# Optimization experiments

Hardware: AMD Instinct MI355X
Metric: run time of the kernel (lower is better)

The kernel has to match this reference:

```python
import jax, jax.numpy as jnp
import numpy as np

B, L1, Q_DIM, V_DIM = 4, 4096, 256, 256
NH, NL, NP = 8, 4, 4
LEVELS = [(128, 128), (64, 64), (32, 32), (16, 16)]
L2 = sum(h * w for h, w in LEVELS)  # 21760


def setup_inputs() -> dict:
    key = jax.random.key(0)
    ks = jax.random.split(key, 12)
    xav = lambda k, so, si: jax.random.normal(k, (so, si), jnp.float32) * np.sqrt(2.0 / (so + si)).astype(np.float32)
    # reference windows: centers in [0.1,0.9], box sizes in [0.05,0.25]
    c = 0.1 + 0.8 * jax.random.uniform(ks[0], (B, L1, 2), jnp.float32)
    s = 0.05 + 0.2 * jax.random.uniform(ks[1], (B, L1, 2), jnp.float32)
    v_shape = jnp.array(LEVELS, dtype=jnp.int32)
    v_start_index = jnp.array(np.cumsum([0] + [h * w for h, w in LEVELS[:-1]]), dtype=jnp.int32)
    return {
        'query': jax.random.normal(ks[2], (B, L1, Q_DIM), jnp.float32),
        'value': jax.random.normal(ks[3], (B, L2, V_DIM), jnp.float32),
        'v_shape': v_shape,
        'v_mask': jnp.zeros((B, L2), jnp.bool_),
        'v_start_index': v_start_index,
        'v_valid_ratios': jnp.ones((B, 1, 1, NL, 1, 2), jnp.float32),
        'ref_windows': jnp.concatenate([c, s], axis=-1),
        'Wo': 0.01 * jax.random.normal(ks[4], (NH * NL * NP * 2, Q_DIM), jnp.float32),
        'bo': 0.5 * jax.random.normal(ks[5], (NH * NL * NP * 2,), jnp.float32),
        'Wa': 0.02 * jax.random.normal(ks[6], (NH * NL * NP, Q_DIM), jnp.float32),
        'ba': jnp.zeros((NH * NL * NP,), jnp.float32),
        'Wv': xav(ks[7], V_DIM, V_DIM),
        'bv': jnp.zeros((V_DIM,), jnp.float32),
        'Wout': xav(ks[8], Q_DIM, V_DIM),
        'bout': jnp.zeros((Q_DIM,), jnp.float32),
    }


def _ms_deform_sample(value, v_shape, v_start, loc):
    """value: (b,l2,h,d); loc: (b,l1,h,L,P,2) in [0,1] -> (b,l1,L,P,h,d).
    Bilinear sampling with zero padding, align_corners=False semantics."""
    b, l2, h, d = value.shape
    _, l1, _, L, P, _ = loc.shape
    Hi = v_shape[:, 0][None, None, None, :, None]  # (1,1,1,L,1) int
    Wi = v_shape[:, 1][None, None, None, :, None]
    x = loc[..., 0] * Wi.astype(loc.dtype) - 0.5  # (b,l1,h,L,P)
    y = loc[..., 1] * Hi.astype(loc.dtype) - 0.5
    x0 = jnp.floor(x)
    y0 = jnp.floor(y)
    lx, ly = x - x0, y - y0
    x0i = x0.astype(jnp.int32)
    y0i = y0.astype(jnp.int32)
    start = v_start[None, None, None, :, None]
    acc = jnp.zeros((b, l1 * L * P, h, d), loc.dtype)
    for dy, wy in ((0, 1.0 - ly), (1, ly)):
        for dx, wx in ((0, 1.0 - lx), (1, lx)):
            xi = x0i + dx
            yi = y0i + dy
            valid = (xi >= 0) & (xi < Wi) & (yi >= 0) & (yi < Hi)
            w = wx * wy * valid.astype(loc.dtype)  # (b,l1,h,L,P)
            xc = jnp.clip(xi, 0, Wi - 1)
            yc = jnp.clip(yi, 0, Hi - 1)
            flat = start + yc * Wi + xc  # (b,l1,h,L,P) index into l2
            flat_t = flat.transpose(0, 1, 3, 4, 2).reshape(b, l1 * L * P, h)
            w_t = w.transpose(0, 1, 3, 4, 2).reshape(b, l1 * L * P, h)
            g = jnp.take_along_axis(value, flat_t[..., None], axis=1)  # (b,M,h,d)
            acc = acc + g * w_t[..., None]
    return acc.reshape(b, l1, L, P, h, d)


def reference(query, value, v_shape, v_mask, v_start_index, v_valid_ratios, ref_windows,
              Wo, bo, Wa, ba, Wv, bv, Wout, bout):
    b, l1, _ = query.shape
    l2 = value.shape[1]
    hd = value.shape[-1] // NH
    v = value @ Wv.T + bv
    v = jnp.where(v_mask[..., None], 0.0, v).reshape(b, l2, NH, hd)
    off = (query @ Wo.T + bo).reshape(b, l1, NH, NL, NP, 2)
    attn = jax.nn.softmax((query @ Wa.T + ba).reshape(b, l1, NH, NL * NP), axis=-1)
    attn = attn.reshape(b, l1, NH, NL, NP)
    loc = ref_windows[:, :, None, None, None, :2] + off / 8.0 * ref_windows[:, :, None, None, None, 2:]
    loc = loc * v_valid_ratios
    sampled = _ms_deform_sample(v, v_shape, v_start_index, loc)  # (b,l1,L,P,h,d)
    out = jnp.einsum('blLPhd,blhLP->blhd', sampled, attn).reshape(b, l1, NH * hd)
    out = out @ Wout.T + bout
    return out, attn
```

## Files before the change

### kernel.cpp

```cpp
#include <hip/hip_runtime.h>
#include <cstdint>
#include <cstddef>


#define L2_LEN 21760
#define BQ_TOT 16384
#define KD     256

typedef __attribute__((ext_vector_type(8))) _Float16 half8;
typedef __attribute__((ext_vector_type(4))) float    f32x4;

__device__ __forceinline__ void glds16(const _Float16* g, _Float16* l) {
    __builtin_amdgcn_global_load_lds(
        (const __attribute__((address_space(1))) void*)g,
        (__attribute__((address_space(3))) void*)l, 16, 0, 0);
}

__global__ __launch_bounds__(256) void cvt_f32_f16(
    const float* __restrict__ in, _Float16* __restrict__ out, int n8)
{
    for (int i = blockIdx.x * 256 + threadIdx.x; i < n8; i += gridDim.x * 256) {
        const float4 f0 = ((const float4*)in)[i * 2];
        const float4 f1 = ((const float4*)in)[i * 2 + 1];
        half8 h;
        h[0] = (_Float16)f0.x; h[1] = (_Float16)f0.y;
        h[2] = (_Float16)f0.z; h[3] = (_Float16)f0.w;
        h[4] = (_Float16)f1.x; h[5] = (_Float16)f1.y;
        h[6] = (_Float16)f1.z; h[7] = (_Float16)f1.w;
        ((half8*)out)[i] = h;
    }
}

__global__ __launch_bounds__(256) void cvt_weights(
    const float* __restrict__ Wv, const float* __restrict__ Wo,
    const float* __restrict__ Wa, const float* __restrict__ Wout,
    const float* __restrict__ bv, const float* __restrict__ bo,
    const float* __restrict__ ba, const float* __restrict__ bout,
    _Float16* __restrict__ Wp, float* __restrict__ bp)
{
    const int gid = blockIdx.x * 256 + threadIdx.x;
    const float* src; int off8;
    if      (gid <  8192) { src = Wv;   off8 = gid;         }
    else if (gid < 16384) { src = Wo;   off8 = gid -  8192; }
    else if (gid < 20480) { src = Wa;   off8 = gid - 16384; }
    else                  { src = Wout; off8 = gid - 20480; }
    const float4 f0 = ((const float4*)src)[off8 * 2];
    const float4 f1 = ((const float4*)src)[off8 * 2 + 1];
    half8 h;
    h[0] = (_Float16)f0.x; h[1] = (_Float16)f0.y;
    h[2] = (_Float16)f0.z; h[3] = (_Float16)f0.w;
    h[4] = (_Float16)f1.x; h[5] = (_Float16)f1.y;
    h[6] = (_Float16)f1.z; h[7] = (_Float16)f1.w;
    ((half8*)Wp)[gid] = h;
    if (gid < 896) {
        float b;
        if      (gid < 256) b = bv[gid];
        else if (gid < 512) b = bo[gid - 256];
        else if (gid < 640) b = ba[gid - 512];
        else                b = bout[gid - 640];
        bp[gid] = b;
    }
}

template<bool OUT_F16>
__global__ __launch_bounds__(256) void gemm_f16(
    const _Float16* __restrict__ A, const _Float16* __restrict__ Wp,
    const float* __restrict__ bp, int wrow0,
    void* __restrict__ Cv, int ldC, const unsigned char* __restrict__ mask)
{
    __shared__ _Float16 As[4096];
    __shared__ _Float16 Bs[4096];

    const int t = threadIdx.x, lane = t & 63, wid = t >> 6;
    const int wm = wid >> 1, wn = wid & 1;
    const int bm = blockIdx.x, bn = blockIdx.y;

    const int u0 = wid * 128 + lane;
    const int u1 = u0 + 64;
    const int ra0 = ((u0 >> 6) << 4) + (u0 & 15), ca0 = ((u0 >> 4) & 3) * 8;
    const int ra1 = ((u1 >> 6) << 4) + (u1 & 15), ca1 = ((u1 >> 4) & 3) * 8;
    const _Float16* Ag0 = A + (size_t)(bm * 128 + ra0) * KD + ca0;
    const _Float16* Ag1 = A + (size_t)(bm * 128 + ra1) * KD + ca1;
    const _Float16* Wg0 = Wp + (size_t)(wrow0 + bn * 128 + ra0) * KD + ca0;
    const _Float16* Wg1 = Wp + (size_t)(wrow0 + bn * 128 + ra1) * KD + ca1;
    _Float16* Ad0 = &As[wid * 1024];
    _Float16* Ad1 = &As[wid * 1024 + 512];
    _Float16* Bd0 = &Bs[wid * 1024];
    _Float16* Bd1 = &Bs[wid * 1024 + 512];

    f32x4 acc[4][4] = {};

    for (int kk = 0; kk < KD; kk += 32) {
        glds16(Ag0 + kk, Ad0);
        glds16(Ag1 + kk, Ad1);
        glds16(Wg0 + kk, Bd0);
        glds16(Wg1 + kk, Bd1);
        __syncthreads();
        half8 ah[4], bh[4];
#pragma unroll
        for (int x = 0; x < 4; ++x) {
            ah[x] = ((const half8*)As)[(wm * 4 + x) * 64 + lane];
            bh[x] = ((const half8*)Bs)[(wn * 4 + x) * 64 + lane];
        }
#pragma unroll
        for (int m = 0; m < 4; ++m)
#pragma unroll
            for (int n = 0; n < 4; ++n)
                acc[m][n] = __builtin_amdgcn_mfma_f32_16x16x32_f16(
                    ah[m], bh[n], acc[m][n], 0, 0, 0);
        __syncthreads();
    }

    const int rb = bm * 128 + wm * 64, cb = bn * 128 + wn * 64;
    const int cl = lane & 15, rl = (lane >> 4) * 4;
    float bias_n[4];
#pragma unroll
    for (int n = 0; n < 4; ++n) bias_n[n] = bp[wrow0 + cb + n * 16 + cl];
#pragma unroll
    for (int m = 0; m < 4; ++m) {
        float mz[4];
#pragma unroll
        for (int r = 0; r < 4; ++r) {
            const int row = rb + m * 16 + rl + r;
            mz[r] = (mask != nullptr && mask[row]) ? 0.0f : 1.0f;
        }
#pragma unroll
        for (int n = 0; n < 4; ++n) {
            const int col = cb + n * 16 + cl;
#pragma unroll
            for (int r = 0; r < 4; ++r) {
                const int row = rb + m * 16 + rl + r;
                const float val = (acc[m][n][r] + bias_n[n]) * mz[r];
                if (OUT_F16) ((_Float16*)Cv)[(size_t)row * ldC + col] = (_Float16)val;
                else         ((float*)Cv)[(size_t)row * ldC + col] = val;
            }
        }
    }
}

__global__ __launch_bounds__(256) void softmax_kernel(
    const float* __restrict__ logits, int stride,
    float* __restrict__ attn, int total)
{
    const int i = blockIdx.x * blockDim.x + threadIdx.x;
    if (i >= total) return;
    const int q = i >> 3, h = i & 7;
    const float4* p = (const float4*)(logits + (size_t)q * stride + h * 16);
    const float4 v0 = p[0], v1 = p[1], v2 = p[2], v3 = p[3];
    float v[16] = {v0.x, v0.y, v0.z, v0.w, v1.x, v1.y, v1.z, v1.w,
                   v2.x, v2.y, v2.z, v2.w, v3.x, v3.y, v3.z, v3.w};
    float m = v[0];
#pragma unroll
    for (int j = 1; j < 16; ++j) m = fmaxf(m, v[j]);
    float s = 0.0f;
#pragma unroll
    for (int j = 0; j < 16; ++j) { v[j] = __expf(v[j] - m); s += v[j]; }
    const float inv = 1.0f / s;
    float4* o = (float4*)(attn + (size_t)i * 16);
    o[0] = make_float4(v[0] * inv, v[1] * inv, v[2] * inv, v[3] * inv);
    o[1] = make_float4(v[4] * inv, v[5] * inv, v[6] * inv, v[7] * inv);
    o[2] = make_float4(v[8] * inv, v[9] * inv, v[10] * inv, v[11] * inv);
    o[3] = make_float4(v[12] * inv, v[13] * inv, v[14] * inv, v[15] * inv);
}

__global__ __launch_bounds__(128) void sample_f16(
    const _Float16* __restrict__ v,
    const float* __restrict__ qp,
    const float* __restrict__ attn,
    const float* __restrict__ ref,
    const float* __restrict__ vr,
    const int*   __restrict__ vshape,
    const int*   __restrict__ vstart,
    _Float16* __restrict__ sout)
{
    const int t  = threadIdx.x;
    const int q  = blockIdx.x * 4 + (t >> 5);
    const int h  = (t >> 2) & 7;
    const int c0 = (t & 3) * 8;
    const int b  = q >> 12;

    const float4 rw = *(const float4*)(ref + (size_t)q * 4);
    const float* op = qp + (size_t)q * 384 + h * 32;
    const float* ap = attn + (size_t)q * 128 + h * 16;

    float acc[8] = {};

#pragma unroll
    for (int l = 0; l < 4; ++l) {
        const int H = vshape[l * 2 + 0];
        const int W = vshape[l * 2 + 1];
        const int start = vstart[l];
        const float vrx = vr[(b * 4 + l) * 2 + 0];
        const float vry = vr[(b * 4 + l) * 2 + 1];
        const float fW = (float)W, fH = (float)H;
        const _Float16* vb = v + ((size_t)b * L2_LEN + start) * 256 + h * 32 + c0;
#pragma unroll
        for (int p = 0; p < 4; ++p) {
            const float a  = ap[l * 4 + p];
            const float ox = op[(l * 4 + p) * 2 + 0];
            const float oy = op[(l * 4 + p) * 2 + 1];
            const float x = (rw.x + ox * 0.125f * rw.z) * vrx * fW - 0.5f;
            const float y = (rw.y + oy * 0.125f * rw.w) * vry * fH - 0.5f;
            const float x0f = floorf(x), y0f = floorf(y);
            const float fx = x - x0f, fy = y - y0f;
            const int x0 = (int)x0f, y0 = (int)y0f;
            const float wx0 = (x0 >= 0 && x0 < W)         ? (1.0f - fx) : 0.0f;
            const float wx1 = (x0 + 1 >= 0 && x0 + 1 < W) ? fx          : 0.0f;
            const float wy0 = (y0 >= 0 && y0 < H)         ? (1.0f - fy) : 0.0f;
            const float wy1 = (y0 + 1 >= 0 && y0 + 1 < H) ? fy          : 0.0f;
            const int xc0 = min(max(x0, 0), W - 1),     xc1 = min(max(x0 + 1, 0), W - 1);
            const int yc0 = min(max(y0, 0), H - 1),     yc1 = min(max(y0 + 1, 0), H - 1);
            const float w00 = wx0 * wy0 * a, w01 = wx1 * wy0 * a;
            const float w10 = wx0 * wy1 * a, w11 = wx1 * wy1 * a;
            const half8 g00 = *(const half8*)(vb + (size_t)(yc0 * W + xc0) * 256);
            const half8 g01 = *(const half8*)(vb + (size_t)(yc0 * W + xc1) * 256);
            const half8 g10 = *(const half8*)(vb + (size_t)(yc1 * W + xc0) * 256);
            const half8 g11 = *(const half8*)(vb + (size_t)(yc1 * W + xc1) * 256);
#pragma unroll
            for (int j = 0; j < 8; ++j)
                acc[j] += w00 * (float)g00[j] + w01 * (float)g01[j]
                        + w10 * (float)g10[j] + w11 * (float)g11[j];
        }
    }

    half8 o;
#pragma unroll
    for (int j = 0; j < 8; ++j) o[j] = (_Float16)acc[j];
    *(half8*)(sout + (size_t)q * 256 + h * 32 + c0) = o;
}

extern "C" void kernel_launch(void* const* d_in, const int* in_sizes, int n_in,
                              void* d_out, int out_size, void* d_ws, size_t ws_size,
                              hipStream_t stream)
{
    const float*         query    = (const float*)d_in[0];
    const float*         value    = (const float*)d_in[1];
    const int*           v_shape  = (const int*)d_in[2];
    const unsigned char* v_mask   = (const unsigned char*)d_in[3];
    const int*           v_start  = (const int*)d_in[4];
    const float*         v_ratios = (const float*)d_in[5];
    const float*         ref_w    = (const float*)d_in[6];
    const float*         Wo       = (const float*)d_in[7];
    const float*         bo       = (const float*)d_in[8];
    const float*         Wa       = (const float*)d_in[9];
    const float*         ba       = (const float*)d_in[10];
    const float*         Wv       = (const float*)d_in[11];
    const float*         bv       = (const float*)d_in[12];
    const float*         Wout     = (const float*)d_in[13];
    const float*         bout     = (const float*)d_in[14];

    float* out      = (float*)d_out;
    float* attn_out = out + (size_t)BQ_TOT * 256;

    _Float16* Vf = (_Float16*)d_ws;
    _Float16* vh = Vf + (size_t)4 * L2_LEN * 256;
    _Float16* Qf = vh + (size_t)4 * L2_LEN * 256;
    _Float16* Sf = Qf + (size_t)BQ_TOT * 256;
    _Float16* Wp = Sf + (size_t)BQ_TOT * 256;
    float*    bp = (float*)(Wp + 229376);
    float*    qp = bp + 896;

    cvt_f32_f16<<<2048, 256, 0, stream>>>(value, Vf, (4 * L2_LEN * 256) / 8);
    cvt_f32_f16<<<2048, 256, 0, stream>>>(query, Qf, (BQ_TOT * 256) / 8);
    cvt_weights<<<112, 256, 0, stream>>>(Wv, Wo, Wa, Wout, bv, bo, ba, bout, Wp, bp);
    gemm_f16<true><<<dim3(680, 2), 256, 0, stream>>>(
        Vf, Wp, bp, 0, vh, 256, v_mask);
    gemm_f16<false><<<dim3(128, 3), 256, 0, stream>>>(
        Qf, Wp, bp, 256, qp, 384, nullptr);
    softmax_kernel<<<512, 256, 0, stream>>>(qp + 256, 384, attn_out, BQ_TOT * 8);
    sample_f16<<<4096, 128, 0, stream>>>(
        vh, qp, attn_out, ref_w, v_ratios, v_shape, v_start, Sf);
    gemm_f16<false><<<dim3(128, 2), 256, 0, stream>>>(
        Sf, Wp, bp, 640, out, 256, nullptr);
}
```

Measured before the change: 292.8 us.

## Fuse f32-to-f16 conversion into GEMMs, fold softmax into sampler, head-major value layout

Result: faster. 274.5 us (-6.3%).

```diff
diff --git a/kernel.cpp b/kernel.cpp
--- a/kernel.cpp
+++ b/kernel.cpp
@@ -5,7 +5,6 @@
 
 #define L2_LEN 21760
 #define BQ_TOT 16384
-#define KD     256
 
 typedef __attribute__((ext_vector_type(8))) _Float16 half8;
 typedef __attribute__((ext_vector_type(4))) float    f32x4;
@@ -15,20 +14,13 @@
         (const __attribute__((address_space(1))) void*)g,
         (__attribute__((address_space(3))) void*)l, 16, 0, 0);
 }
-
-__global__ __launch_bounds__(256) void cvt_f32_f16(
-    const float* __restrict__ in, _Float16* __restrict__ out, int n8)
-{
-    for (int i = blockIdx.x * 256 + threadIdx.x; i < n8; i += gridDim.x * 256) {
-        const float4 f0 = ((const float4*)in)[i * 2];
-        const float4 f1 = ((const float4*)in)[i * 2 + 1];
-        half8 h;
-        h[0] = (_Float16)f0.x; h[1] = (_Float16)f0.y;
-        h[2] = (_Float16)f0.z; h[3] = (_Float16)f0.w;
-        h[4] = (_Float16)f1.x; h[5] = (_Float16)f1.y;
-        h[6] = (_Float16)f1.z; h[7] = (_Float16)f1.w;
-        ((half8*)out)[i] = h;
-    }
+__device__ __forceinline__ half8 cvt8(float4 a, float4 b) {
+    half8 h;
+    h[0] = (_Float16)a.x; h[1] = (_Float16)a.y;
+    h[2] = (_Float16)a.z; h[3] = (_Float16)a.w;
+    h[4] = (_Float16)b.x; h[5] = (_Float16)b.y;
+    h[6] = (_Float16)b.z; h[7] = (_Float16)b.w;
+    return h;
 }
 
 __global__ __launch_bounds__(256) void cvt_weights(
@@ -46,12 +38,7 @@
     else                  { src = Wout; off8 = gid - 20480; }
     const float4 f0 = ((const float4*)src)[off8 * 2];
     const float4 f1 = ((const float4*)src)[off8 * 2 + 1];
-    half8 h;
-    h[0] = (_Float16)f0.x; h[1] = (_Float16)f0.y;
-    h[2] = (_Float16)f0.z; h[3] = (_Float16)f0.w;
-    h[4] = (_Float16)f1.x; h[5] = (_Float16)f1.y;
-    h[6] = (_Float16)f1.z; h[7] = (_Float16)f1.w;
-    ((half8*)Wp)[gid] = h;
+    ((half8*)Wp)[gid] = cvt8(f0, f1);
     if (gid < 896) {
         float b;
         if      (gid < 256) b = bv[gid];
@@ -62,11 +49,84 @@
     }
 }
 
-template<bool OUT_F16>
-__global__ __launch_bounds__(256) void gemm_f16(
-    const _Float16* __restrict__ A, const _Float16* __restrict__ Wp,
+__global__ __launch_bounds__(512) void gemm_vproj(
+    const float* __restrict__ A,
+    const _Float16* __restrict__ Wp,
+    const float* __restrict__ bp,
+    _Float16* __restrict__ vh,
+    const unsigned char* __restrict__ mask)
+{
+    __shared__ _Float16 As[4096];
+    __shared__ _Float16 Bs[8192];
+
+    const int t = threadIdx.x, lane = t & 63, wid = t >> 6;
+    const int wm = wid >> 2, wn = wid & 3;
+    const int bm = blockIdx.x;
+
+    const int ar = t >> 2, akp = t & 3;
+    const float* Ag = A + (size_t)(bm * 128 + ar) * 256 + akp * 8;
+    _Float16* Ad = &As[((ar >> 4) * 64 + akp * 16 + (ar & 15)) * 8];
+
+    const int u0 = wid * 128 + lane, u1 = u0 + 64;
+    const int br0 = ((u0 >> 6) << 4) + (u0 & 15), bk0 = ((u0 >> 4) & 3) * 8;
+    const int br1 = ((u1 >> 6) << 4) + (u1 & 15), bk1 = ((u1 >> 4) & 3) * 8;
+    const _Float16* Wg0 = Wp + (size_t)br0 * 256 + bk0;
+    const _Float16* Wg1 = Wp + (size_t)br1 * 256 + bk1;
+    _Float16* Bd0 = &Bs[(size_t)wid * 1024];
+    _Float16* Bd1 = Bd0 + 512;
+
+    f32x4 acc[4][4] = {};
+
+    for (int kk = 0; kk < 256; kk += 32) {
+        const float4 a0 = *(const float4*)(Ag + kk);
+        const float4 a1 = *(const float4*)(Ag + kk + 4);
+        __syncthreads();
+        glds16(Wg0 + kk, Bd0);
+        glds16(Wg1 + kk, Bd1);
+        *(half8*)Ad = cvt8(a0, a1);
+        __syncthreads();
+        half8 ah[4], bh[4];
+#pragma unroll
+        for (int x = 0; x < 4; ++x) {
+            ah[x] = ((const half8*)As)[(wm * 4 + x) * 64 + lane];
+            bh[x] = ((const half8*)Bs)[(wn * 4 + x) * 64 + lane];
+        }
+#pragma unroll
+        for (int m = 0; m < 4; ++m)
+#pragma unroll
+            for (int n = 0; n < 4; ++n)
+                acc[m][n] = __builtin_amdgcn_mfma_f32_16x16x32_f16(
+                    ah[m], bh[n], acc[m][n], 0, 0, 0);
+    }
+
+    const int b = bm / 170;
+    const int l2b = (bm - b * 170) * 128;
+    const int cl = lane & 15, rl = (lane >> 4) * 4;
+#pragma unroll
+    for (int m = 0; m < 4; ++m) {
+        const int ro = wm * 64 + m * 16 + rl;
+        float mz[4];
+#pragma unroll
+        for (int r = 0; r < 4; ++r)
+            mz[r] = mask[bm * 128 + ro + r] ? 0.0f : 1.0f;
+#pragma unroll
+        for (int n = 0; n < 4; ++n) {
+            const int col = wn * 64 + n * 16 + cl;
+            const int h = col >> 5, c = col & 31;
+            const float bb = bp[col];
+            _Float16* dst = vh + ((size_t)(b * 8 + h) * L2_LEN + l2b + ro) * 32 + c;
+#pragma unroll
+            for (int r = 0; r < 4; ++r)
+                dst[(size_t)r * 32] = (_Float16)((acc[m][n][r] + bb) * mz[r]);
+        }
+    }
+}
+
+template<bool A_F32>
+__global__ __launch_bounds__(256) void gemm_qo(
+    const void* __restrict__ Av, const _Float16* __restrict__ Wp,
     const float* __restrict__ bp, int wrow0,
-    void* __restrict__ Cv, int ldC, const unsigned char* __restrict__ mask)
+    float* __restrict__ C, int ldC)
 {
     __shared__ _Float16 As[4096];
     __shared__ _Float16 Bs[4096];
@@ -75,26 +135,47 @@
     const int wm = wid >> 1, wn = wid & 1;
     const int bm = blockIdx.x, bn = blockIdx.y;
 
-    const int u0 = wid * 128 + lane;
-    const int u1 = u0 + 64;
-    const int ra0 = ((u0 >> 6) << 4) + (u0 & 15), ca0 = ((u0 >> 4) & 3) * 8;
-    const int ra1 = ((u1 >> 6) << 4) + (u1 & 15), ca1 = ((u1 >> 4) & 3) * 8;
-    const _Float16* Ag0 = A + (size_t)(bm * 128 + ra0) * KD + ca0;
-    const _Float16* Ag1 = A + (size_t)(bm * 128 + ra1) * KD + ca1;
-    const _Float16* Wg0 = Wp + (size_t)(wrow0 + bn * 128 + ra0) * KD + ca0;
-    const _Float16* Wg1 = Wp + (size_t)(wrow0 + bn * 128 + ra1) * KD + ca1;
-    _Float16* Ad0 = &As[wid * 1024];
-    _Float16* Ad1 = &As[wid * 1024 + 512];
-    _Float16* Bd0 = &Bs[wid * 1024];
-    _Float16* Bd1 = &Bs[wid * 1024 + 512];
+    const int u0 = wid * 128 + lane, u1 = u0 + 64;
+    const int br0 = ((u0 >> 6) << 4) + (u0 & 15), bk0 = ((u0 >> 4) & 3) * 8;
+    const int br1 = ((u1 >> 6) << 4) + (u1 & 15), bk1 = ((u1 >> 4) & 3) * 8;
+    const _Float16* Wg0 = Wp + (size_t)(wrow0 + bn * 128 + br0) * 256 + bk0;
+    const _Float16* Wg1 = Wp + (size_t)(wrow0 + bn * 128 + br1) * 256 + bk1;
+    _Float16* Bd0 = &Bs[(size_t)wid * 1024];
+    _Float16* Bd1 = Bd0 + 512;
+
+    const float*    Agf = nullptr; _Float16* Adf0 = nullptr; _Float16* Adf1 = nullptr;
+    const _Float16* Agh0 = nullptr; const _Float16* Agh1 = nullptr;
+    _Float16* Adh0 = nullptr; _Float16* Adh1 = nullptr;
+    if (A_F32) {
+        const int r = t >> 1, kp = (t & 1) * 2;
+        Agf  = (const float*)Av + (size_t)(bm * 128 + r) * 256 + kp * 8;
+        Adf0 = &As[((r >> 4) * 64 + kp * 16 + (r & 15)) * 8];
+        Adf1 = Adf0 + 128;
+    } else {
+        Agh0 = (const _Float16*)Av + (size_t)(bm * 128 + br0) * 256 + bk0;
+        Agh1 = (const _Float16*)Av + (size_t)(bm * 128 + br1) * 256 + bk1;
+        Adh0 = &As[(size_t)wid * 1024];
+        Adh1 = Adh0 + 512;
+    }
 
     f32x4 acc[4][4] = {};
 
-    for (int kk = 0; kk < KD; kk += 32) {
-        glds16(Ag0 + kk, Ad0);
-        glds16(Ag1 + kk, Ad1);
+    for (int kk = 0; kk < 256; kk += 32) {
+        float4 a0, a1, a2, a3;
+        if (A_F32) {
+            a0 = *(const float4*)(Agf + kk);      a1 = *(const float4*)(Agf + kk + 4);
+            a2 = *(const float4*)(Agf + kk + 8);  a3 = *(const float4*)(Agf + kk + 12);
+        }
+        __syncthreads();
         glds16(Wg0 + kk, Bd0);
         glds16(Wg1 + kk, Bd1);
+        if (A_F32) {
+            *(half8*)Adf0 = cvt8(a0, a1);
+            *(half8*)Adf1 = cvt8(a2, a3);
+        } else {
+            glds16(Agh0 + kk, Adh0);
+            glds16(Agh1 + kk, Adh1);
+        }
         __syncthreads();
         half8 ah[4], bh[4];
 #pragma unroll
@@ -108,114 +189,95 @@
             for (int n = 0; n < 4; ++n)
                 acc[m][n] = __builtin_amdgcn_mfma_f32_16x16x32_f16(
                     ah[m], bh[n], acc[m][n], 0, 0, 0);
-        __syncthreads();
     }
 
     const int rb = bm * 128 + wm * 64, cb = bn * 128 + wn * 64;
     const int cl = lane & 15, rl = (lane >> 4) * 4;
-    float bias_n[4];
-#pragma unroll
-    for (int n = 0; n < 4; ++n) bias_n[n] = bp[wrow0 + cb + n * 16 + cl];
-#pragma unroll
-    for (int m = 0; m < 4; ++m) {
-        float mz[4];
-#pragma unroll
-        for (int r = 0; r < 4; ++r) {
-            const int row = rb + m * 16 + rl + r;
-            mz[r] = (mask != nullptr && mask[row]) ? 0.0f : 1.0f;
-        }
-#pragma unroll
-        for (int n = 0; n < 4; ++n) {
-            const int col = cb + n * 16 + cl;
-#pragma unroll
-            for (int r = 0; r < 4; ++r) {
-                const int row = rb + m * 16 + rl + r;
-                const float val = (acc[m][n][r] + bias_n[n]) * mz[r];
-                if (OUT_F16) ((_Float16*)Cv)[(size_t)row * ldC + col] = (_Float16)val;
-                else         ((float*)Cv)[(size_t)row * ldC + col] = val;
-            }
-        }
-    }
-}
-
-__global__ __launch_bounds__(256) void softmax_kernel(
-    const float* __restrict__ logits, int stride,
-    float* __restrict__ attn, int total)
-{
-    const int i = blockIdx.x * blockDim.x + threadIdx.x;
-    if (i >= total) return;
-    const int q = i >> 3, h = i & 7;
-    const float4* p = (const float4*)(logits + (size_t)q * stride + h * 16);
-    const float4 v0 = p[0], v1 = p[1], v2 = p[2], v3 = p[3];
-    float v[16] = {v0.x, v0.y, v0.z, v0.w, v1.x, v1.y, v1.z, v1.w,
-                   v2.x, v2.y, v2.z, v2.w, v3.x, v3.y, v3.z, v3.w};
-    float m = v[0];
-#pragma unroll
-    for (int j = 1; j < 16; ++j) m = fmaxf(m, v[j]);
-    float s = 0.0f;
-#pragma unroll
-    for (int j = 0; j < 16; ++j) { v[j] = __expf(v[j] - m); s += v[j]; }
-    const float inv = 1.0f / s;
-    float4* o = (float4*)(attn + (size_t)i * 16);
-    o[0] = make_float4(v[0] * inv, v[1] * inv, v[2] * inv, v[3] * inv);
-    o[1] = make_float4(v[4] * inv, v[5] * inv, v[6] * inv, v[7] * inv);
-    o[2] = make_float4(v[8] * inv, v[9] * inv, v[10] * inv, v[11] * inv);
-    o[3] = make_float4(v[12] * inv, v[13] * inv, v[14] * inv, v[15] * inv);
-}
-
-__global__ __launch_bounds__(128) void sample_f16(
+#pragma unroll
+    for (int n = 0; n < 4; ++n) {
+        const float bb = bp[wrow0 + cb + n * 16 + cl];
+#pragma unroll
+        for (int m = 0; m < 4; ++m)
+#pragma unroll
+            for (int r = 0; r < 4; ++r)
+                C[(size_t)(rb + m * 16 + rl + r) * ldC + cb + n * 16 + cl] =
+                    acc[m][n][r] + bb;
+    }
+}
+
+__global__ __launch_bounds__(128) void sample_fused(
     const _Float16* __restrict__ v,
     const float* __restrict__ qp,
-    const float* __restrict__ attn,
     const float* __restrict__ ref,
     const float* __restrict__ vr,
-    const int*   __restrict__ vshape,
-    const int*   __restrict__ vstart,
+    float* __restrict__ attn_out,
     _Float16* __restrict__ sout)
 {
+    constexpr int HH[4] = {128, 64, 32, 16};
+    constexpr int SS[4] = {0, 16384, 20480, 21504};
+
     const int t  = threadIdx.x;
     const int q  = blockIdx.x * 4 + (t >> 5);
     const int h  = (t >> 2) & 7;
     const int c0 = (t & 3) * 8;
     const int b  = q >> 12;
 
+    const float* lg = qp + (size_t)q * 384 + 256 + h * 16;
+    const float4 l0 = ((const float4*)lg)[0], l1 = ((const float4*)lg)[1];
+    const float4 l2 = ((const float4*)lg)[2], l3 = ((const float4*)lg)[3];
+    float ap[16] = {l0.x, l0.y, l0.z, l0.w, l1.x, l1.y, l1.z, l1.w,
+                    l2.x, l2.y, l2.z, l2.w, l3.x, l3.y, l3.z, l3.w};
+    float mx = ap[0];
+#pragma unroll
+    for (int j = 1; j < 16; ++j) mx = fmaxf(mx, ap[j]);
+    float sum = 0.0f;
+#pragma unroll
+    for (int j = 0; j < 16; ++j) { ap[j] = __expf(ap[j] - mx); sum += ap[j]; }
+    const float inv = 1.0f / sum;
+#pragma unroll
+    for (int j = 0; j < 16; ++j) ap[j] *= inv;
+    if (c0 == 0) {
+        float4* ao = (float4*)(attn_out + ((size_t)q * 8 + h) * 16);
+        ao[0] = make_float4(ap[0], ap[1], ap[2], ap[3]);
+        ao[1] = make_float4(ap[4], ap[5], ap[6], ap[7]);
+        ao[2] = make_float4(ap[8], ap[9], ap[10], ap[11]);
+        ao[3] = make_float4(ap[12], ap[13], ap[14], ap[15]);
+    }
+
     const float4 rw = *(const float4*)(ref + (size_t)q * 4);
     const float* op = qp + (size_t)q * 384 + h * 32;
-    const float* ap = attn + (size_t)q * 128 + h * 16;
 
     float acc[8] = {};
 
 #pragma unroll
     for (int l = 0; l < 4; ++l) {
-        const int H = vshape[l * 2 + 0];
-        const int W = vshape[l * 2 + 1];
-        const int start = vstart[l];
+        const int HW = HH[l];
+        const float fHW = (float)HW;
         const float vrx = vr[(b * 4 + l) * 2 + 0];
         const float vry = vr[(b * 4 + l) * 2 + 1];
-        const float fW = (float)W, fH = (float)H;
-        const _Float16* vb = v + ((size_t)b * L2_LEN + start) * 256 + h * 32 + c0;
+        const _Float16* vb = v + ((size_t)(b * 8 + h) * L2_LEN + SS[l]) * 32 + c0;
 #pragma unroll
         for (int p = 0; p < 4; ++p) {
             const float a  = ap[l * 4 + p];
             const float ox = op[(l * 4 + p) * 2 + 0];
             const float oy = op[(l * 4 + p) * 2 + 1];
-            const float x = (rw.x + ox * 0.125f * rw.z) * vrx * fW - 0.5f;
-            const float y = (rw.y + oy * 0.125f * rw.w) * vry * fH - 0.5f;
+            const float x = (rw.x + ox * 0.125f * rw.z) * vrx * fHW - 0.5f;
+            const float y = (rw.y + oy * 0.125f * rw.w) * vry * fHW - 0.5f;
             const float x0f = floorf(x), y0f = floorf(y);
             const float fx = x - x0f, fy = y - y0f;
             const int x0 = (int)x0f, y0 = (int)y0f;
-            const float wx0 = (x0 >= 0 && x0 < W)         ? (1.0f - fx) : 0.0f;
-            const float wx1 = (x0 + 1 >= 0 && x0 + 1 < W) ? fx          : 0.0f;
-            const float wy0 = (y0 >= 0 && y0 < H)         ? (1.0f - fy) : 0.0f;
-            const float wy1 = (y0 + 1 >= 0 && y0 + 1 < H) ? fy          : 0.0f;
-            const int xc0 = min(max(x0, 0), W - 1),     xc1 = min(max(x0 + 1, 0), W - 1);
-            const int yc0 = min(max(y0, 0), H - 1),     yc1 = min(max(y0 + 1, 0), H - 1);
+            const float wx0 = (x0 >= 0 && x0 < HW)         ? (1.0f - fx) : 0.0f;
+            const float wx1 = (x0 + 1 >= 0 && x0 + 1 < HW) ? fx          : 0.0f;
+            const float wy0 = (y0 >= 0 && y0 < HW)         ? (1.0f - fy) : 0.0f;
+            const float wy1 = (y0 + 1 >= 0 && y0 + 1 < HW) ? fy          : 0.0f;
+            const int xc0 = min(max(x0, 0), HW - 1), xc1 = min(max(x0 + 1, 0), HW - 1);
+            const int yc0 = min(max(y0, 0), HW - 1), yc1 = min(max(y0 + 1, 0), HW - 1);
             const float w00 = wx0 * wy0 * a, w01 = wx1 * wy0 * a;
             const float w10 = wx0 * wy1 * a, w11 = wx1 * wy1 * a;
-            const half8 g00 = *(const half8*)(vb + (size_t)(yc0 * W + xc0) * 256);
-            const half8 g01 = *(const half8*)(vb + (size_t)(yc0 * W + xc1) * 256);
-            const half8 g10 = *(const half8*)(vb + (size_t)(yc1 * W + xc0) * 256);
-            const half8 g11 = *(const half8*)(vb + (size_t)(yc1 * W + xc1) * 256);
+            const half8 g00 = *(const half8*)(vb + (size_t)(yc0 * HW + xc0) * 32);
+            const half8 g01 = *(const half8*)(vb + (size_t)(yc0 * HW + xc1) * 32);
+            const half8 g10 = *(const half8*)(vb + (size_t)(yc1 * HW + xc0) * 32);
+            const half8 g11 = *(const half8*)(vb + (size_t)(yc1 * HW + xc1) * 32);
 #pragma unroll
             for (int j = 0; j < 8; ++j)
                 acc[j] += w00 * (float)g00[j] + w01 * (float)g01[j]
@@ -235,9 +297,7 @@
 {
     const float*         query    = (const float*)d_in[0];
     const float*         value    = (const float*)d_in[1];
-    const int*           v_shape  = (const int*)d_in[2];
     const unsigned char* v_mask   = (const unsigned char*)d_in[3];
-    const int*           v_start  = (const int*)d_in[4];
     const float*         v_ratios = (const float*)d_in[5];
     const float*         ref_w    = (const float*)d_in[6];
     const float*         Wo       = (const float*)d_in[7];
@@ -252,24 +312,15 @@
     float* out      = (float*)d_out;
     float* attn_out = out + (size_t)BQ_TOT * 256;
 
-    _Float16* Vf = (_Float16*)d_ws;
-    _Float16* vh = Vf + (size_t)4 * L2_LEN * 256;
-    _Float16* Qf = vh + (size_t)4 * L2_LEN * 256;
-    _Float16* Sf = Qf + (size_t)BQ_TOT * 256;
-    _Float16* Wp = Sf + (size_t)BQ_TOT * 256;
-    float*    bp = (float*)(Wp + 229376);
+    _Float16* Wp = (_Float16*)d_ws;
+    float*    bp = (float*)(Wp + 896 * 256);
     float*    qp = bp + 896;
-
-    cvt_f32_f16<<<2048, 256, 0, stream>>>(value, Vf, (4 * L2_LEN * 256) / 8);
-    cvt_f32_f16<<<2048, 256, 0, stream>>>(query, Qf, (BQ_TOT * 256) / 8);
+    _Float16* vh = (_Float16*)(qp + (size_t)BQ_TOT * 384);
+    _Float16* Sf = vh + (size_t)4 * L2_LEN * 256;
+
     cvt_weights<<<112, 256, 0, stream>>>(Wv, Wo, Wa, Wout, bv, bo, ba, bout, Wp, bp);
-    gemm_f16<true><<<dim3(680, 2), 256, 0, stream>>>(
-        Vf, Wp, bp, 0, vh, 256, v_mask);
-    gemm_f16<false><<<dim3(128, 3), 256, 0, stream>>>(
-        Qf, Wp, bp, 256, qp, 384, nullptr);
-    softmax_kernel<<<512, 256, 0, stream>>>(qp + 256, 384, attn_out, BQ_TOT * 8);
-    sample_f16<<<4096, 128, 0, stream>>>(
-        vh, qp, attn_out, ref_w, v_ratios, v_shape, v_start, Sf);
-    gemm_f16<false><<<dim3(128, 2), 256, 0, stream>>>(
-        Sf, Wp, bp, 640, out, 256, nullptr);
-}
+    gemm_vproj<<<680, 512, 0, stream>>>(value, Wp, bp, vh, v_mask);
+    gemm_qo<true><<<dim3(128, 3), 256, 0, stream>>>(query, Wp, bp, 256, qp, 384);
+    sample_fused<<<4096, 128, 0, stream>>>(vh, qp, ref_w, v_ratios, attn_out, Sf);
+    gemm_qo<false><<<dim3(128, 2), 256, 0, stream>>>(Sf, Wp, bp, 640, out, 256);
+}
```
